# Kernel optimization log

Hardware: AMD Instinct MI355X
Metric: run time of the kernel (lower is better)

## Reference

```python
import jax, jax.numpy as jnp
import numpy as np

N = 50000   # nodes
E = 600000  # edges
F = 128     # num_features
H = 128     # hidden_channels
G = 64      # graphs in batch


def setup_inputs() -> dict:
    key = jax.random.key(0)
    ks = jax.random.split(key, 12)
    x = jax.random.normal(ks[0], (N, F), dtype=jnp.float32)
    edge_index = jax.random.randint(ks[1], (2, E), 0, N, dtype=jnp.int64)
    edge_mask = jax.random.randint(ks[2], (E,), 0, 3, dtype=jnp.int64)
    batch = jnp.sort(jax.random.randint(ks[3], (N,), 0, G, dtype=jnp.int64))
    s = 0.05
    W1 = jax.random.normal(ks[4], (F, H), dtype=jnp.float32) * s
    b1 = jnp.zeros((H,), jnp.float32)
    W2 = jax.random.normal(ks[5], (H, H), dtype=jnp.float32) * s
    b2 = jnp.zeros((H,), jnp.float32)
    W3 = jax.random.normal(ks[6], (H, H), dtype=jnp.float32) * s
    b3 = jnp.zeros((H,), jnp.float32)
    Wl = jax.random.normal(ks[7], (H, 1), dtype=jnp.float32) * s
    bl = jnp.zeros((1,), jnp.float32)
    return {"x": x, "edge_index": edge_index, "edge_mask": edge_mask, "batch": batch,
            "W1": W1, "b1": b1, "W2": W2, "b2": b2, "W3": W3, "b3": b3, "Wl": Wl, "bl": bl}


def gcn_conv(x, W, b, src, dst, ew, n):
    """PyG GCNConv: add self-loops, symmetric deg^-1/2 normalization.
    ew is a {0,1} per-edge weight implementing the dynamic edge subset
    (equivalent to edge_index[:, idx] subsetting, since masked edges
    contribute neither to degree nor to aggregation)."""
    h = x @ W                                                # [n, H]
    deg = jax.ops.segment_sum(ew, dst, num_segments=n) + 1.0  # self-loop adds 1
    dinv = jax.lax.rsqrt(deg)                                # deg^-1/2
    norm = ew * dinv[src] * dinv[dst]                        # per-edge coeff
    agg = jax.ops.segment_sum(h[src] * norm[:, None], dst, num_segments=n)
    agg = agg + h * (dinv * dinv)[:, None]                   # self-loop term 1/deg_i
    return agg + b


def reference(x, edge_index, edge_mask, batch, W1, b1, W2, b2, W3, b3, Wl, bl):
    src, dst = edge_index[0], edge_index[1]
    ones = jnp.ones((E,), x.dtype)
    h = jax.nn.relu(gcn_conv(x, W1, b1, src, dst, ones, N))
    m1 = (edge_mask == 1).astype(x.dtype)
    h = jax.nn.relu(gcn_conv(h, W2, b2, src, dst, m1, N))
    m2 = (edge_mask == 2).astype(x.dtype)
    h = gcn_conv(h, W3, b3, src, dst, m2, N)
    # global_mean_pool over batch ids
    sums = jax.ops.segment_sum(h, batch, num_segments=G)        # [G, H]
    cnt = jax.ops.segment_sum(jnp.ones((N,), h.dtype), batch, num_segments=G)
    pooled = sums / jnp.clip(cnt, 1.0)[:, None]
    # dropout(p=0.3) is identity in eval mode
    return pooled @ Wl + bl
```

## Files before the change

### kernel.cpp

```cpp
#include <hip/hip_runtime.h>

#define NN 50000
#define EE 600000
#define HH 128
#define GG 64
#define NPAD 50176
#define NR 196
#define RN 256
#define NSEC3 150528
#define NBLK3 588
#define EPB 3072
#define SCAP 3584
#define STAGB 7168

typedef __attribute__((ext_vector_type(8))) short short8;
typedef __attribute__((ext_vector_type(4))) float f32x4;
typedef __attribute__((ext_vector_type(4))) unsigned int u32x4;

__device__ __forceinline__ float bf2f(unsigned int u16) {
    union { unsigned int i; float f; } v; v.i = u16 << 16; return v.f;
}
__device__ __forceinline__ unsigned short f2bf(float f) {
    union { float f; unsigned int i; } v; v.f = f;
    unsigned int u = v.i;
    return (unsigned short)((u + 0x7FFFu + ((u >> 16) & 1u)) >> 16);
}

__device__ __forceinline__ short8 cvt8(f32x4 lo, f32x4 hi) {
    short8 r;
    r[0] = (short)f2bf(lo[0]); r[1] = (short)f2bf(lo[1]);
    r[2] = (short)f2bf(lo[2]); r[3] = (short)f2bf(lo[3]);
    r[4] = (short)f2bf(hi[0]); r[5] = (short)f2bf(hi[1]);
    r[6] = (short)f2bf(hi[2]); r[7] = (short)f2bf(hi[3]);
    return r;
}

__global__ __launch_bounds__(256) void k_part(const int* __restrict__ ei, const int* __restrict__ mask,
                                              int* __restrict__ scnt, unsigned int* __restrict__ sbuf) {
    __shared__ int bcnt[256];
    __shared__ int bcur[256];
    __shared__ int gbase[256];
    int t = threadIdx.x;
    int e0 = blockIdx.x * EPB;
    unsigned int pk[12]; int bin[12];
    bcnt[t] = 0; bcur[t] = 0;
    __syncthreads();
    #pragma unroll
    for (int j = 0; j < 12; j++) {
        int e = e0 + j * 256 + t;
        if (e < EE) {
            int s = ei[e];
            int d = ei[EE + e];
            int m = mask[e];
            pk[j] = (unsigned int)s | ((unsigned int)(d & 255) << 16) | ((unsigned int)m << 24);
            bin[j] = d >> 8;
            atomicAdd(&bcnt[bin[j]], 1);
        } else bin[j] = -1;
    }
    __syncthreads();
    int v = bcnt[t];
    gbase[t] = (v > 0) ? atomicAdd(&scnt[t], v) : 0;
    __syncthreads();
    #pragma unroll
    for (int j = 0; j < 12; j++) {
        if (bin[j] >= 0) {
            int b = bin[j];
            int pos = gbase[b] + atomicAdd(&bcur[b], 1);
            if (pos < SCAP) sbuf[(size_t)b * SCAP + pos] = pk[j];
        }
    }
}

__global__ __launch_bounds__(256) void k_cnt(const int* __restrict__ scnt,
                                             const unsigned int* __restrict__ sbuf,
                                             int* __restrict__ deg, float* __restrict__ dinv) {
    __shared__ int l0[RN], l1[RN], l2[RN];
    int t = threadIdx.x;
    int rng = blockIdx.x;
    l0[t] = 0; l1[t] = 0; l2[t] = 0;
    __syncthreads();
    int cnt = scnt[rng]; if (cnt > SCAP) cnt = SCAP;
    const unsigned int* sb = sbuf + (size_t)rng * SCAP;
    for (int i = t; i < cnt; i += 256) {
        unsigned int p = sb[i];
        int dl = (int)((p >> 16) & 255u);
        int m = (int)(p >> 24);
        atomicAdd(&l0[dl], 1);
        if (m == 1) atomicAdd(&l1[dl], 1);
        else if (m == 2) atomicAdd(&l2[dl], 1);
    }
    __syncthreads();
    int node = rng * RN + t;
    int a = l0[t], b = l1[t], c = l2[t];
    deg[node] = a;
    deg[NPAD + node] = b;
    deg[2 * NPAD + node] = c;
    dinv[node] = rsqrtf((float)a + 1.0f);
    dinv[NPAD + node] = rsqrtf((float)b + 1.0f);
    dinv[2 * NPAD + node] = rsqrtf((float)c + 1.0f);
}

__global__ __launch_bounds__(256) void k_scan1(const int* __restrict__ deg, int* __restrict__ btot) {
    __shared__ int ws[4];
    int t = threadIdx.x, lane = t & 63, w = t >> 6;
    int v = deg[blockIdx.x * 256 + t];
    #pragma unroll
    for (int off = 32; off > 0; off >>= 1) v += __shfl_xor(v, off);
    if (lane == 0) ws[w] = v;
    __syncthreads();
    if (t == 0) btot[blockIdx.x] = ws[0] + ws[1] + ws[2] + ws[3];
}

__global__ __launch_bounds__(1024) void k_scan2(const int* __restrict__ btot, int* __restrict__ boff) {
    __shared__ int ws[16];
    int t = threadIdx.x, lane = t & 63, w = t >> 6;
    int v = (t < NBLK3) ? btot[t] : 0;
    int x = v;
    #pragma unroll
    for (int off = 1; off < 64; off <<= 1) {
        int u = __shfl_up(x, off);
        if (lane >= off) x += u;
    }
    if (lane == 63) ws[w] = x;
    __syncthreads();
    int wo = 0;
    for (int k = 0; k < w; k++) wo += ws[k];
    if (t < NBLK3) boff[t] = wo + x - v;
}

__global__ __launch_bounds__(256) void k_scan3(const int* __restrict__ deg, const int* __restrict__ boff,
                                               int* __restrict__ rp) {
    __shared__ int ws[4];
    int t = threadIdx.x, lane = t & 63, w = t >> 6;
    int i = blockIdx.x * 256 + t;
    int v = deg[i];
    int x = v;
    #pragma unroll
    for (int off = 1; off < 64; off <<= 1) {
        int u = __shfl_up(x, off);
        if (lane >= off) x += u;
    }
    if (lane == 63) ws[w] = x;
    __syncthreads();
    int wo = 0;
    for (int k = 0; k < w; k++) wo += ws[k];
    int r = boff[blockIdx.x] + wo + x - v;
    rp[i] = r;
    if (i == NSEC3 - 1) rp[NSEC3] = r + v;
}

__global__ __launch_bounds__(256) void k_build(const int* __restrict__ scnt,
                                               const unsigned int* __restrict__ sbuf,
                                               const int* __restrict__ rp,
                                               unsigned short* __restrict__ csr) {
    __shared__ int lrp0[RN + 1], lrp1[RN + 1], lrp2[RN + 1];
    __shared__ int lc0[RN], lc1[RN], lc2[RN];
    __shared__ unsigned short stag[STAGB];
    int t = threadIdx.x;
    int rng = blockIdx.x;
    int vd0 = rng * RN;
    int base0 = rp[vd0], base1 = rp[NPAD + vd0], base2 = rp[2 * NPAD + vd0];
    for (int i = t; i < RN + 1; i += 256) {
        lrp0[i] = rp[vd0 + i] - base0;
        lrp1[i] = rp[NPAD + vd0 + i] - base1;
        lrp2[i] = rp[2 * NPAD + vd0 + i] - base2;
    }
    lc0[t] = 0; lc1[t] = 0; lc2[t] = 0;
    __syncthreads();
    int c0 = lrp0[RN], c1 = lrp1[RN], c2 = lrp2[RN];
    int cnt = scnt[rng]; if (cnt > SCAP) cnt = SCAP;
    const unsigned int* sb = sbuf + (size_t)rng * SCAP;
    for (int i = t; i < cnt; i += 256) {
        unsigned int p = sb[i];
        unsigned short src = (unsigned short)(p & 0xffffu);
        int dl = (int)((p >> 16) & 255u);
        int m = (int)(p >> 24);
        int sl = lrp0[dl] + atomicAdd(&lc0[dl], 1);
        stag[sl] = src;
        if (m == 1) { sl = c0 + lrp1[dl] + atomicAdd(&lc1[dl], 1); stag[sl] = src; }
        else if (m == 2) { sl = c0 + c1 + lrp2[dl] + atomicAdd(&lc2[dl], 1); stag[sl] = src; }
    }
    __syncthreads();
    for (int i = t; i < c0; i += 256) csr[base0 + i] = stag[i];
    for (int i = t; i < c1; i += 256) csr[base1 + i] = stag[c0 + i];
    for (int i = t; i < c2; i += 256) csr[base2 + i] = stag[c0 + c1 + i];
}

__global__ void k_wt3(const float* __restrict__ W1, const float* __restrict__ W2,
                      const float* __restrict__ W3, unsigned short* __restrict__ wt) {
    int i = blockIdx.x * 256 + threadIdx.x;
    int which = i >> 14;
    int r = i & 16383;
    const float* w = (which == 0) ? W1 : (which == 1) ? W2 : W3;
    int k = r >> 7, n = r & 127;
    wt[which * 16384 + n * HH + k] = f2bf(w[r]);
}

__global__ __launch_bounds__(256) void k_gemm_f(const float* __restrict__ in,
                                                const unsigned short* __restrict__ wt,
                                                unsigned short* __restrict__ h) {
    int w = threadIdx.x >> 6, lane = threadIdx.x & 63;
    int lr = lane & 15, lg = lane >> 4;
    int rowbase = (blockIdx.x * 4 + w) * 16;
    if (rowbase >= NN) return;
    int arow = rowbase + lr;
    const f32x4* ap = (const f32x4*)(in + (size_t)arow * HH + lg * 8);
    short8 a0 = cvt8(ap[0], ap[1]);
    short8 a1 = cvt8(ap[8], ap[9]);
    short8 a2 = cvt8(ap[16], ap[17]);
    short8 a3 = cvt8(ap[24], ap[25]);
    f32x4 acc[8];
    #pragma unroll
    for (int i = 0; i < 8; i++) acc[i] = (f32x4){0.f, 0.f, 0.f, 0.f};
    const unsigned short* wbase = wt + lr * HH + lg * 8;
    #pragma unroll
    for (int nc = 0; nc < 8; nc++) {
        const short8* bp = (const short8*)(wbase + nc * 16 * HH);
        short8 b0 = bp[0], b1 = bp[4], b2 = bp[8], b3 = bp[12];
        acc[nc] = __builtin_amdgcn_mfma_f32_16x16x32_bf16(a0, b0, acc[nc], 0, 0, 0);
        acc[nc] = __builtin_amdgcn_mfma_f32_16x16x32_bf16(a1, b1, acc[nc], 0, 0, 0);
        acc[nc] = __builtin_amdgcn_mfma_f32_16x16x32_bf16(a2, b2, acc[nc], 0, 0, 0);
        acc[nc] = __builtin_amdgcn_mfma_f32_16x16x32_bf16(a3, b3, acc[nc], 0, 0, 0);
    }
    int orow = rowbase + lg * 4;
    #pragma unroll
    for (int nc = 0; nc < 8; nc++) {
        #pragma unroll
        for (int j = 0; j < 4; j++) {
            h[(size_t)(orow + j) * HH + nc * 16 + lr] = f2bf(acc[nc][j]);
        }
    }
}

__global__ __launch_bounds__(256) void k_gemm_b(const unsigned short* __restrict__ in,
                                                const unsigned short* __restrict__ wt,
                                                unsigned short* __restrict__ h) {
    int w = threadIdx.x >> 6, lane = threadIdx.x & 63;
    int lr = lane & 15, lg = lane >> 4;
    int rowbase = (blockIdx.x * 4 + w) * 16;
    if (rowbase >= NN) return;
    int arow = rowbase + lr;
    const short8* ap = (const short8*)(in + (size_t)arow * HH + lg * 8);
    short8 a0 = ap[0], a1 = ap[4], a2 = ap[8], a3 = ap[12];
    f32x4 acc[8];
    #pragma unroll
    for (int i = 0; i < 8; i++) acc[i] = (f32x4){0.f, 0.f, 0.f, 0.f};
    const unsigned short* wbase = wt + lr * HH + lg * 8;
    #pragma unroll
    for (int nc = 0; nc < 8; nc++) {
        const short8* bp = (const short8*)(wbase + nc * 16 * HH);
        short8 b0 = bp[0], b1 = bp[4], b2 = bp[8], b3 = bp[12];
        acc[nc] = __builtin_amdgcn_mfma_f32_16x16x32_bf16(a0, b0, acc[nc], 0, 0, 0);
        acc[nc] = __builtin_amdgcn_mfma_f32_16x16x32_bf16(a1, b1, acc[nc], 0, 0, 0);
        acc[nc] = __builtin_amdgcn_mfma_f32_16x16x32_bf16(a2, b2, acc[nc], 0, 0, 0);
        acc[nc] = __builtin_amdgcn_mfma_f32_16x16x32_bf16(a3, b3, acc[nc], 0, 0, 0);
    }
    int orow = rowbase + lg * 4;
    #pragma unroll
    for (int nc = 0; nc < 8; nc++) {
        #pragma unroll
        for (int j = 0; j < 4; j++) {
            h[(size_t)(orow + j) * HH + nc * 16 + lr] = f2bf(acc[nc][j]);
        }
    }
}

__global__ __launch_bounds__(256) void k_agg(const unsigned short* __restrict__ h,
                                             const float* __restrict__ dinv,
                                             const unsigned short* __restrict__ csr,
                                             const int* __restrict__ rp,
                                             const float* __restrict__ bias,
                                             unsigned short* __restrict__ g,
                                             int relu) {
    int tid = threadIdx.x;
    int n = blockIdx.x * 16 + (tid >> 4);
    int l = tid & 15;
    float di = dinv[n];
    float c = di * di;
    u32x4 hv = *(const u32x4*)(h + (size_t)n * HH + l * 8);
    float acc0 = bf2f(hv[0] & 0xffffu) * c, acc1 = bf2f(hv[0] >> 16) * c;
    float acc2 = bf2f(hv[1] & 0xffffu) * c, acc3 = bf2f(hv[1] >> 16) * c;
    float acc4 = bf2f(hv[2] & 0xffffu) * c, acc5 = bf2f(hv[2] >> 16) * c;
    float acc6 = bf2f(hv[3] & 0xffffu) * c, acc7 = bf2f(hv[3] >> 16) * c;
    int e = rp[n], end = rp[n + 1];
    for (; e + 1 < end; e += 2) {
        int s0 = (int)csr[e];
        int s1 = (int)csr[e + 1];
        float w0 = dinv[s0] * di;
        float w1 = dinv[s1] * di;
        u32x4 v0 = *(const u32x4*)(h + (size_t)s0 * HH + l * 8);
        u32x4 v1 = *(const u32x4*)(h + (size_t)s1 * HH + l * 8);
        acc0 += w0 * bf2f(v0[0] & 0xffffu); acc1 += w0 * bf2f(v0[0] >> 16);
        acc2 += w0 * bf2f(v0[1] & 0xffffu); acc3 += w0 * bf2f(v0[1] >> 16);
        acc4 += w0 * bf2f(v0[2] & 0xffffu); acc5 += w0 * bf2f(v0[2] >> 16);
        acc6 += w0 * bf2f(v0[3] & 0xffffu); acc7 += w0 * bf2f(v0[3] >> 16);
        acc0 += w1 * bf2f(v1[0] & 0xffffu); acc1 += w1 * bf2f(v1[0] >> 16);
        acc2 += w1 * bf2f(v1[1] & 0xffffu); acc3 += w1 * bf2f(v1[1] >> 16);
        acc4 += w1 * bf2f(v1[2] & 0xffffu); acc5 += w1 * bf2f(v1[2] >> 16);
        acc6 += w1 * bf2f(v1[3] & 0xffffu); acc7 += w1 * bf2f(v1[3] >> 16);
    }
    if (e < end) {
        int s0 = (int)csr[e];
        float w0 = dinv[s0] * di;
        u32x4 v0 = *(const u32x4*)(h + (size_t)s0 * HH + l * 8);
        acc0 += w0 * bf2f(v0[0] & 0xffffu); acc1 += w0 * bf2f(v0[0] >> 16);
        acc2 += w0 * bf2f(v0[1] & 0xffffu); acc3 += w0 * bf2f(v0[1] >> 16);
        acc4 += w0 * bf2f(v0[2] & 0xffffu); acc5 += w0 * bf2f(v0[2] >> 16);
        acc6 += w0 * bf2f(v0[3] & 0xffffu); acc7 += w0 * bf2f(v0[3] >> 16);
    }
    f32x4 bp0 = *(const f32x4*)(bias + l * 8);
    f32x4 bp1 = *(const f32x4*)(bias + l * 8 + 4);
    acc0 += bp0[0]; acc1 += bp0[1]; acc2 += bp0[2]; acc3 += bp0[3];
    acc4 += bp1[0]; acc5 += bp1[1]; acc6 += bp1[2]; acc7 += bp1[3];
    if (relu) {
        acc0 = fmaxf(acc0, 0.f); acc1 = fmaxf(acc1, 0.f);
        acc2 = fmaxf(acc2, 0.f); acc3 = fmaxf(acc3, 0.f);
        acc4 = fmaxf(acc4, 0.f); acc5 = fmaxf(acc5, 0.f);
        acc6 = fmaxf(acc6, 0.f); acc7 = fmaxf(acc7, 0.f);
    }
    u32x4 o;
    o[0] = (unsigned int)f2bf(acc0) | ((unsigned int)f2bf(acc1) << 16);
    o[1] = (unsigned int)f2bf(acc2) | ((unsigned int)f2bf(acc3) << 16);
    o[2] = (unsigned int)f2bf(acc4) | ((unsigned int)f2bf(acc5) << 16);
    o[3] = (unsigned int)f2bf(acc6) | ((unsigned int)f2bf(acc7) << 16);
    *(u32x4*)(g + (size_t)n * HH + l * 8) = o;
}

__global__ __launch_bounds__(128) void k_pool_part(const unsigned short* __restrict__ g3,
                                                   const int* __restrict__ batch,
                                                   float* __restrict__ sums) {
    int t = threadIdx.x;
    int n0 = blockIdx.x * 64;
    int n1 = n0 + 64; if (n1 > NN) n1 = NN;
    int curb = batch[n0];
    float acc = 0.f;
    for (int n = n0; n < n1; n++) {
        int b = batch[n];
        if (b != curb) {
            atomicAdd(&sums[curb * HH + t], acc);
            acc = 0.f;
            curb = b;
        }
        acc += bf2f((unsigned int)g3[(size_t)n * HH + t]);
    }
    atomicAdd(&sums[curb * HH + t], acc);
}

__device__ __forceinline__ int lbound(const int* a, int n, int key) {
    int lo = 0, hi = n;
    while (lo < hi) { int mid = (lo + hi) >> 1; if (a[mid] < key) lo = mid + 1; else hi = mid; }
    return lo;
}

__global__ __launch_bounds__(128) void k_head(const float* __restrict__ sums,
                                              const int* __restrict__ batch,
                                              const float* __restrict__ Wl,
                                              const float* __restrict__ bl,
                                              float* __restrict__ out) {
    int gid = blockIdx.x;
    int t = threadIdx.x;
    int lo = lbound(batch, NN, gid);
    int hi = lbound(batch, NN, gid + 1);
    float cnt = (float)(hi - lo);
    if (cnt < 1.f) cnt = 1.f;
    float prod = (sums[gid * HH + t] / cnt) * Wl[t];
    __shared__ float sm[128];
    sm[t] = prod;
    __syncthreads();
    for (int off = 64; off > 0; off >>= 1) {
        if (t < off) sm[t] += sm[t + off];
        __syncthreads();
    }
    if (t == 0) out[gid] = sm[0] + bl[0];
}

extern "C" void kernel_launch(void* const* d_in, const int* in_sizes, int n_in,
                              void* d_out, int out_size, void* d_ws, size_t ws_size,
                              hipStream_t stream) {
    const float* x    = (const float*)d_in[0];
    const int*   ei   = (const int*)d_in[1];
    const int*   mask = (const int*)d_in[2];
    const int*   batch= (const int*)d_in[3];
    const float* W1   = (const float*)d_in[4];
    const float* b1   = (const float*)d_in[5];
    const float* W2   = (const float*)d_in[6];
    const float* b2   = (const float*)d_in[7];
    const float* W3   = (const float*)d_in[8];
    const float* b3   = (const float*)d_in[9];
    const float* Wl   = (const float*)d_in[10];
    const float* bl   = (const float*)d_in[11];
    float* out = (float*)d_out;

    char* ws = (char*)d_ws;
    unsigned short* g = (unsigned short*)(ws + 0);
    unsigned short* h = (unsigned short*)(ws + 12800000);
    unsigned short* wt1 = (unsigned short*)(ws + 25600000);
    unsigned short* wt2 = wt1 + 16384;
    unsigned short* wt3 = wt2 + 16384;
    int* deg   = (int*)(ws + 25698304);
    float* dinv= (float*)(ws + 26300416);
    int* rp    = (int*)(ws + 26902528);
    int* btot  = (int*)(ws + 27505152);
    int* boff  = (int*)(ws + 27509248);
    int* scnt  = (int*)(ws + 27513344);
    unsigned short* csr = (unsigned short*)(ws + 27514368);
    unsigned int* sbuf = (unsigned int*)(ws + 29914368);
    float* sums = (float*)(ws + 32724224);

    float* dinv1 = dinv;
    float* dinv2 = dinv + NPAD;
    float* dinv3 = dinv + 2 * NPAD;

    hipMemsetAsync(scnt, 0, (size_t)NR * sizeof(int), stream);
    hipMemsetAsync(sums, 0, (size_t)GG * HH * sizeof(float), stream);

    dim3 b256(256);
    k_part<<<dim3((EE + EPB - 1) / EPB), b256, 0, stream>>>(ei, mask, scnt, sbuf);
    k_cnt<<<dim3(NR), b256, 0, stream>>>(scnt, sbuf, deg, dinv);
    k_scan1<<<dim3(NBLK3), b256, 0, stream>>>(deg, btot);
    k_scan2<<<dim3(1), dim3(1024), 0, stream>>>(btot, boff);
    k_scan3<<<dim3(NBLK3), b256, 0, stream>>>(deg, boff, rp);
    k_build<<<dim3(NR), b256, 0, stream>>>(scnt, sbuf, rp, csr);

    k_wt3<<<dim3(192), b256, 0, stream>>>(W1, W2, W3, wt1);

    dim3 ggrid((NN + 63) / 64);
    dim3 agrid(NN / 16);

    k_gemm_f<<<ggrid, b256, 0, stream>>>(x, wt1, h);
    k_agg<<<agrid, b256, 0, stream>>>(h, dinv1, csr, rp, b1, g, 1);
    k_gemm_b<<<ggrid, b256, 0, stream>>>(g, wt2, h);
    k_agg<<<agrid, b256, 0, stream>>>(h, dinv2, csr, rp + NPAD, b2, g, 1);
    k_gemm_b<<<ggrid, b256, 0, stream>>>(g, wt3, h);
    k_agg<<<agrid, b256, 0, stream>>>(h, dinv3, csr, rp + 2 * NPAD, b3, g, 0);

    k_pool_part<<<dim3((NN + 63) / 64), dim3(128), 0, stream>>>(g, batch, sums);
    k_head<<<dim3(GG), dim3(128), 0, stream>>>(sums, batch, Wl, bl, out);
}
```

Baseline: 197.2 us.

## Fuse CSR scans into count/build kernels and fuse last aggregation with pooling

Range totals are now reduced inside k_cnt and the per-node exclusive scan is done inside k_build, which replaces three scan kernels with one small scan over range totals. The final aggregation now accumulates into pooled sums through shared-memory atomics, which removes the bf16 write of layer-3 output and the separate pooling kernel. Zeroing of sums moves into the weight-transpose kernel, which drops a memset. The edge loop is unrolled by 4 to issue more gathers in flight, at the cost of more registers and a heavier atomic epilogue.

```diff
diff --git a/kernel.cpp b/kernel.cpp
--- a/kernel.cpp
+++ b/kernel.cpp
@@ -8,7 +8,7 @@
 #define NR 196
 #define RN 256
 #define NSEC3 150528
-#define NBLK3 588
+#define NRT 588
 #define EPB 3072
 #define SCAP 3584
 #define STAGB 7168
@@ -73,9 +73,11 @@
 
 __global__ __launch_bounds__(256) void k_cnt(const int* __restrict__ scnt,
                                              const unsigned int* __restrict__ sbuf,
-                                             int* __restrict__ deg, float* __restrict__ dinv) {
+                                             int* __restrict__ deg, float* __restrict__ dinv,
+                                             int* __restrict__ rtot) {
     __shared__ int l0[RN], l1[RN], l2[RN];
-    int t = threadIdx.x;
+    __shared__ int red[12];
+    int t = threadIdx.x, lane = t & 63, w = t >> 6;
     int rng = blockIdx.x;
     l0[t] = 0; l1[t] = 0; l2[t] = 0;
     __syncthreads();
@@ -98,23 +100,22 @@
     dinv[node] = rsqrtf((float)a + 1.0f);
     dinv[NPAD + node] = rsqrtf((float)b + 1.0f);
     dinv[2 * NPAD + node] = rsqrtf((float)c + 1.0f);
-}
-
-__global__ __launch_bounds__(256) void k_scan1(const int* __restrict__ deg, int* __restrict__ btot) {
-    __shared__ int ws[4];
-    int t = threadIdx.x, lane = t & 63, w = t >> 6;
-    int v = deg[blockIdx.x * 256 + t];
-    #pragma unroll
-    for (int off = 32; off > 0; off >>= 1) v += __shfl_xor(v, off);
-    if (lane == 0) ws[w] = v;
-    __syncthreads();
-    if (t == 0) btot[blockIdx.x] = ws[0] + ws[1] + ws[2] + ws[3];
-}
-
-__global__ __launch_bounds__(1024) void k_scan2(const int* __restrict__ btot, int* __restrict__ boff) {
+    int sa = a, sb_ = b, sc = c;
+    #pragma unroll
+    for (int off = 32; off > 0; off >>= 1) {
+        sa += __shfl_xor(sa, off); sb_ += __shfl_xor(sb_, off); sc += __shfl_xor(sc, off);
+    }
+    if (lane == 0) { red[w] = sa; red[4 + w] = sb_; red[8 + w] = sc; }
+    __syncthreads();
+    if (t == 0) rtot[rng] = red[0] + red[1] + red[2] + red[3];
+    else if (t == 1) rtot[NR + rng] = red[4] + red[5] + red[6] + red[7];
+    else if (t == 2) rtot[2 * NR + rng] = red[8] + red[9] + red[10] + red[11];
+}
+
+__global__ __launch_bounds__(1024) void k_scanR(const int* __restrict__ rtot, int* __restrict__ roff) {
     __shared__ int ws[16];
     int t = threadIdx.x, lane = t & 63, w = t >> 6;
-    int v = (t < NBLK3) ? btot[t] : 0;
+    int v = (t < NRT) ? rtot[t] : 0;
     int x = v;
     #pragma unroll
     for (int off = 1; off < 64; off <<= 1) {
@@ -125,47 +126,41 @@
     __syncthreads();
     int wo = 0;
     for (int k = 0; k < w; k++) wo += ws[k];
-    if (t < NBLK3) boff[t] = wo + x - v;
-}
-
-__global__ __launch_bounds__(256) void k_scan3(const int* __restrict__ deg, const int* __restrict__ boff,
-                                               int* __restrict__ rp) {
-    __shared__ int ws[4];
-    int t = threadIdx.x, lane = t & 63, w = t >> 6;
-    int i = blockIdx.x * 256 + t;
-    int v = deg[i];
-    int x = v;
-    #pragma unroll
-    for (int off = 1; off < 64; off <<= 1) {
-        int u = __shfl_up(x, off);
-        if (lane >= off) x += u;
-    }
-    if (lane == 63) ws[w] = x;
-    __syncthreads();
-    int wo = 0;
-    for (int k = 0; k < w; k++) wo += ws[k];
-    int r = boff[blockIdx.x] + wo + x - v;
-    rp[i] = r;
-    if (i == NSEC3 - 1) rp[NSEC3] = r + v;
+    if (t < NRT) roff[t] = wo + x - v;
 }
 
 __global__ __launch_bounds__(256) void k_build(const int* __restrict__ scnt,
                                                const unsigned int* __restrict__ sbuf,
-                                               const int* __restrict__ rp,
+                                               const int* __restrict__ deg,
+                                               const int* __restrict__ roff,
+                                               int* __restrict__ rp,
                                                unsigned short* __restrict__ csr) {
     __shared__ int lrp0[RN + 1], lrp1[RN + 1], lrp2[RN + 1];
     __shared__ int lc0[RN], lc1[RN], lc2[RN];
+    __shared__ int wsum[12];
     __shared__ unsigned short stag[STAGB];
-    int t = threadIdx.x;
+    int t = threadIdx.x, lane = t & 63, w = t >> 6;
     int rng = blockIdx.x;
     int vd0 = rng * RN;
-    int base0 = rp[vd0], base1 = rp[NPAD + vd0], base2 = rp[2 * NPAD + vd0];
-    for (int i = t; i < RN + 1; i += 256) {
-        lrp0[i] = rp[vd0 + i] - base0;
-        lrp1[i] = rp[NPAD + vd0 + i] - base1;
-        lrp2[i] = rp[2 * NPAD + vd0 + i] - base2;
-    }
+    int d0 = deg[vd0 + t], d1 = deg[NPAD + vd0 + t], d2 = deg[2 * NPAD + vd0 + t];
+    int x0 = d0, x1 = d1, x2 = d2;
+    #pragma unroll
+    for (int off = 1; off < 64; off <<= 1) {
+        int u0 = __shfl_up(x0, off), u1 = __shfl_up(x1, off), u2 = __shfl_up(x2, off);
+        if (lane >= off) { x0 += u0; x1 += u1; x2 += u2; }
+    }
+    if (lane == 63) { wsum[w] = x0; wsum[4 + w] = x1; wsum[8 + w] = x2; }
+    __syncthreads();
+    int wo0 = 0, wo1 = 0, wo2 = 0;
+    for (int k = 0; k < w; k++) { wo0 += wsum[k]; wo1 += wsum[4 + k]; wo2 += wsum[8 + k]; }
+    int e0 = wo0 + x0 - d0, e1 = wo1 + x1 - d1, e2 = wo2 + x2 - d2;
+    lrp0[t] = e0; lrp1[t] = e1; lrp2[t] = e2;
+    if (t == 255) { lrp0[RN] = e0 + d0; lrp1[RN] = e1 + d1; lrp2[RN] = e2 + d2; }
     lc0[t] = 0; lc1[t] = 0; lc2[t] = 0;
+    int base0 = roff[rng], base1 = roff[NR + rng], base2 = roff[2 * NR + rng];
+    rp[vd0 + t] = base0 + e0;
+    rp[NPAD + vd0 + t] = base1 + e1;
+    rp[2 * NPAD + vd0 + t] = base2 + e2;
     __syncthreads();
     int c0 = lrp0[RN], c1 = lrp1[RN], c2 = lrp2[RN];
     int cnt = scnt[rng]; if (cnt > SCAP) cnt = SCAP;
@@ -186,9 +181,11 @@
     for (int i = t; i < c2; i += 256) csr[base2 + i] = stag[c0 + c1 + i];
 }
 
-__global__ void k_wt3(const float* __restrict__ W1, const float* __restrict__ W2,
-                      const float* __restrict__ W3, unsigned short* __restrict__ wt) {
+__global__ void k_wt3z(const float* __restrict__ W1, const float* __restrict__ W2,
+                       const float* __restrict__ W3, unsigned short* __restrict__ wt,
+                       float* __restrict__ sums) {
     int i = blockIdx.x * 256 + threadIdx.x;
+    if (i < GG * HH) sums[i] = 0.f;
     int which = i >> 14;
     int r = i & 16383;
     const float* w = (which == 0) ? W1 : (which == 1) ? W2 : W3;
@@ -265,85 +262,117 @@
     }
 }
 
+__device__ __forceinline__ void agg_edges(const unsigned short* __restrict__ h,
+                                          const float* __restrict__ dinv,
+                                          const unsigned short* __restrict__ csr,
+                                          int e, int end, float di, int l, float* acc) {
+    for (; e + 3 < end; e += 4) {
+        int s0 = (int)csr[e], s1 = (int)csr[e + 1], s2 = (int)csr[e + 2], s3 = (int)csr[e + 3];
+        float w0 = dinv[s0] * di, w1 = dinv[s1] * di, w2 = dinv[s2] * di, w3 = dinv[s3] * di;
+        u32x4 v0 = *(const u32x4*)(h + (size_t)s0 * HH + l * 8);
+        u32x4 v1 = *(const u32x4*)(h + (size_t)s1 * HH + l * 8);
+        u32x4 v2 = *(const u32x4*)(h + (size_t)s2 * HH + l * 8);
+        u32x4 v3 = *(const u32x4*)(h + (size_t)s3 * HH + l * 8);
+        #pragma unroll
+        for (int q = 0; q < 4; q++) {
+            acc[2*q]   += w0 * bf2f(v0[q] & 0xffffu); acc[2*q+1] += w0 * bf2f(v0[q] >> 16);
+            acc[2*q]   += w1 * bf2f(v1[q] & 0xffffu); acc[2*q+1] += w1 * bf2f(v1[q] >> 16);
+            acc[2*q]   += w2 * bf2f(v2[q] & 0xffffu); acc[2*q+1] += w2 * bf2f(v2[q] >> 16);
+            acc[2*q]   += w3 * bf2f(v3[q] & 0xffffu); acc[2*q+1] += w3 * bf2f(v3[q] >> 16);
+        }
+    }
+    for (; e < end; e++) {
+        int s0 = (int)csr[e];
+        float w0 = dinv[s0] * di;
+        u32x4 v0 = *(const u32x4*)(h + (size_t)s0 * HH + l * 8);
+        #pragma unroll
+        for (int q = 0; q < 4; q++) {
+            acc[2*q]   += w0 * bf2f(v0[q] & 0xffffu); acc[2*q+1] += w0 * bf2f(v0[q] >> 16);
+        }
+    }
+}
+
 __global__ __launch_bounds__(256) void k_agg(const unsigned short* __restrict__ h,
                                              const float* __restrict__ dinv,
                                              const unsigned short* __restrict__ csr,
                                              const int* __restrict__ rp,
                                              const float* __restrict__ bias,
-                                             unsigned short* __restrict__ g,
-                                             int relu) {
+                                             unsigned short* __restrict__ g) {
     int tid = threadIdx.x;
     int n = blockIdx.x * 16 + (tid >> 4);
     int l = tid & 15;
     float di = dinv[n];
     float c = di * di;
     u32x4 hv = *(const u32x4*)(h + (size_t)n * HH + l * 8);
-    float acc0 = bf2f(hv[0] & 0xffffu) * c, acc1 = bf2f(hv[0] >> 16) * c;
-    float acc2 = bf2f(hv[1] & 0xffffu) * c, acc3 = bf2f(hv[1] >> 16) * c;
-    float acc4 = bf2f(hv[2] & 0xffffu) * c, acc5 = bf2f(hv[2] >> 16) * c;
-    float acc6 = bf2f(hv[3] & 0xffffu) * c, acc7 = bf2f(hv[3] >> 16) * c;
-    int e = rp[n], end = rp[n + 1];
-    for (; e + 1 < end; e += 2) {
-        int s0 = (int)csr[e];
-        int s1 = (int)csr[e + 1];
-        float w0 = dinv[s0] * di;
-        float w1 = dinv[s1] * di;
-        u32x4 v0 = *(const u32x4*)(h + (size_t)s0 * HH + l * 8);
-        u32x4 v1 = *(const u32x4*)(h + (size_t)s1 * HH + l * 8);
-        acc0 += w0 * bf2f(v0[0] & 0xffffu); acc1 += w0 * bf2f(v0[0] >> 16);
-        acc2 += w0 * bf2f(v0[1] & 0xffffu); acc3 += w0 * bf2f(v0[1] >> 16);
-        acc4 += w0 * bf2f(v0[2] & 0xffffu); acc5 += w0 * bf2f(v0[2] >> 16);
-        acc6 += w0 * bf2f(v0[3] & 0xffffu); acc7 += w0 * bf2f(v0[3] >> 16);
-        acc0 += w1 * bf2f(v1[0] & 0xffffu); acc1 += w1 * bf2f(v1[0] >> 16);
-        acc2 += w1 * bf2f(v1[1] & 0xffffu); acc3 += w1 * bf2f(v1[1] >> 16);
-        acc4 += w1 * bf2f(v1[2] & 0xffffu); acc5 += w1 * bf2f(v1[2] >> 16);
-        acc6 += w1 * bf2f(v1[3] & 0xffffu); acc7 += w1 * bf2f(v1[3] >> 16);
-    }
-    if (e < end) {
-        int s0 = (int)csr[e];
-        float w0 = dinv[s0] * di;
-        u32x4 v0 = *(const u32x4*)(h + (size_t)s0 * HH + l * 8);
-        acc0 += w0 * bf2f(v0[0] & 0xffffu); acc1 += w0 * bf2f(v0[0] >> 16);
-        acc2 += w0 * bf2f(v0[1] & 0xffffu); acc3 += w0 * bf2f(v0[1] >> 16);
-        acc4 += w0 * bf2f(v0[2] & 0xffffu); acc5 += w0 * bf2f(v0[2] >> 16);
-        acc6 += w0 * bf2f(v0[3] & 0xffffu); acc7 += w0 * bf2f(v0[3] >> 16);
-    }
+    float acc[8];
+    #pragma unroll
+    for (int q = 0; q < 4; q++) {
+        acc[2*q] = bf2f(hv[q] & 0xffffu) * c;
+        acc[2*q+1] = bf2f(hv[q] >> 16) * c;
+    }
+    agg_edges(h, dinv, csr, rp[n], rp[n + 1], di, l, acc);
     f32x4 bp0 = *(const f32x4*)(bias + l * 8);
     f32x4 bp1 = *(const f32x4*)(bias + l * 8 + 4);
-    acc0 += bp0[0]; acc1 += bp0[1]; acc2 += bp0[2]; acc3 += bp0[3];
-    acc4 += bp1[0]; acc5 += bp1[1]; acc6 += bp1[2]; acc7 += bp1[3];
-    if (relu) {
-        acc0 = fmaxf(acc0, 0.f); acc1 = fmaxf(acc1, 0.f);
-        acc2 = fmaxf(acc2, 0.f); acc3 = fmaxf(acc3, 0.f);
-        acc4 = fmaxf(acc4, 0.f); acc5 = fmaxf(acc5, 0.f);
-        acc6 = fmaxf(acc6, 0.f); acc7 = fmaxf(acc7, 0.f);
-    }
+    acc[0] += bp0[0]; acc[1] += bp0[1]; acc[2] += bp0[2]; acc[3] += bp0[3];
+    acc[4] += bp1[0]; acc[5] += bp1[1]; acc[6] += bp1[2]; acc[7] += bp1[3];
+    #pragma unroll
+    for (int q = 0; q < 8; q++) acc[q] = fmaxf(acc[q], 0.f);
     u32x4 o;
-    o[0] = (unsigned int)f2bf(acc0) | ((unsigned int)f2bf(acc1) << 16);
-    o[1] = (unsigned int)f2bf(acc2) | ((unsigned int)f2bf(acc3) << 16);
-    o[2] = (unsigned int)f2bf(acc4) | ((unsigned int)f2bf(acc5) << 16);
-    o[3] = (unsigned int)f2bf(acc6) | ((unsigned int)f2bf(acc7) << 16);
+    #pragma unroll
+    for (int q = 0; q < 4; q++)
+        o[q] = (unsigned int)f2bf(acc[2*q]) | ((unsigned int)f2bf(acc[2*q+1]) << 16);
     *(u32x4*)(g + (size_t)n * HH + l * 8) = o;
 }
 
-__global__ __launch_bounds__(128) void k_pool_part(const unsigned short* __restrict__ g3,
-                                                   const int* __restrict__ batch,
-                                                   float* __restrict__ sums) {
-    int t = threadIdx.x;
-    int n0 = blockIdx.x * 64;
-    int n1 = n0 + 64; if (n1 > NN) n1 = NN;
-    int curb = batch[n0];
-    float acc = 0.f;
-    for (int n = n0; n < n1; n++) {
-        int b = batch[n];
-        if (b != curb) {
-            atomicAdd(&sums[curb * HH + t], acc);
-            acc = 0.f;
-            curb = b;
-        }
-        acc += bf2f((unsigned int)g3[(size_t)n * HH + t]);
-    }
-    atomicAdd(&sums[curb * HH + t], acc);
+__global__ __launch_bounds__(256) void k_aggpool(const unsigned short* __restrict__ h,
+                                                 const float* __restrict__ dinv,
+                                                 const unsigned short* __restrict__ csr,
+                                                 const int* __restrict__ rp,
+                                                 const float* __restrict__ bias,
+                                                 const int* __restrict__ batch,
+                                                 float* __restrict__ sums) {
+    __shared__ float lsum[4][HH];
+    __shared__ int lflag[4];
+    int tid = threadIdx.x;
+    int n = blockIdx.x * 16 + (tid >> 4);
+    int l = tid & 15;
+    for (int i = tid; i < 4 * HH; i += 256) ((float*)lsum)[i] = 0.f;
+    if (tid < 4) lflag[tid] = 0;
+    __syncthreads();
+    float di = dinv[n];
+    float c = di * di;
+    u32x4 hv = *(const u32x4*)(h + (size_t)n * HH + l * 8);
+    float acc[8];
+    #pragma unroll
+    for (int q = 0; q < 4; q++) {
+        acc[2*q] = bf2f(hv[q] & 0xffffu) * c;
+        acc[2*q+1] = bf2f(hv[q] >> 16) * c;
+    }
+    agg_edges(h, dinv, csr, rp[n], rp[n + 1], di, l, acc);
+    f32x4 bp0 = *(const f32x4*)(bias + l * 8);
+    f32x4 bp1 = *(const f32x4*)(bias + l * 8 + 4);
+    acc[0] += bp0[0]; acc[1] += bp0[1]; acc[2] += bp0[2]; acc[3] += bp0[3];
+    acc[4] += bp1[0]; acc[5] += bp1[1]; acc[6] += bp1[2]; acc[7] += bp1[3];
+    int b0 = batch[blockIdx.x * 16];
+    int bn = batch[n];
+    int rel = bn - b0;
+    if (rel < 4) {
+        lflag[rel] = 1;
+        #pragma unroll
+        for (int q = 0; q < 8; q++) atomicAdd(&lsum[rel][l * 8 + q], acc[q]);
+    } else {
+        #pragma unroll
+        for (int q = 0; q < 8; q++) atomicAdd(&sums[bn * HH + l * 8 + q], acc[q]);
+    }
+    __syncthreads();
+    #pragma unroll
+    for (int r = 0; r < 4; r++) {
+        if (lflag[r]) {
+            int gi = b0 + r;
+            for (int i = tid; i < HH; i += 256)
+                atomicAdd(&sums[gi * HH + i], lsum[r][i]);
+        }
+    }
 }
 
 __device__ __forceinline__ int lbound(const int* a, int n, int key) {
@@ -400,8 +429,8 @@
     int* deg   = (int*)(ws + 25698304);
     float* dinv= (float*)(ws + 26300416);
     int* rp    = (int*)(ws + 26902528);
-    int* btot  = (int*)(ws + 27505152);
-    int* boff  = (int*)(ws + 27509248);
+    int* rtot  = (int*)(ws + 27505152);
+    int* roff  = (int*)(ws + 27509248);
     int* scnt  = (int*)(ws + 27513344);
     unsigned short* csr = (unsigned short*)(ws + 27514368);
     unsigned int* sbuf = (unsigned int*)(ws + 29914368);
@@ -412,28 +441,24 @@
     float* dinv3 = dinv + 2 * NPAD;
 
     hipMemsetAsync(scnt, 0, (size_t)NR * sizeof(int), stream);
-    hipMemsetAsync(sums, 0, (size_t)GG * HH * sizeof(float), stream);
 
     dim3 b256(256);
     k_part<<<dim3((EE + EPB - 1) / EPB), b256, 0, stream>>>(ei, mask, scnt, sbuf);
-    k_cnt<<<dim3(NR), b256, 0, stream>>>(scnt, sbuf, deg, dinv);
-    k_scan1<<<dim3(NBLK3), b256, 0, stream>>>(deg, btot);
-    k_scan2<<<dim3(1), dim3(1024), 0, stream>>>(btot, boff);
-    k_scan3<<<dim3(NBLK3), b256, 0, stream>>>(deg, boff, rp);
-    k_build<<<dim3(NR), b256, 0, stream>>>(scnt, sbuf, rp, csr);
-
-    k_wt3<<<dim3(192), b256, 0, stream>>>(W1, W2, W3, wt1);
+    k_cnt<<<dim3(NR), b256, 0, stream>>>(scnt, sbuf, deg, dinv, rtot);
+    k_scanR<<<dim3(1), dim3(1024), 0, stream>>>(rtot, roff);
+    k_build<<<dim3(NR), b256, 0, stream>>>(scnt, sbuf, deg, roff, rp, csr);
+
+    k_wt3z<<<dim3(192), b256, 0, stream>>>(W1, W2, W3, wt1, sums);
 
     dim3 ggrid((NN + 63) / 64);
     dim3 agrid(NN / 16);
 
     k_gemm_f<<<ggrid, b256, 0, stream>>>(x, wt1, h);
-    k_agg<<<agrid, b256, 0, stream>>>(h, dinv1, csr, rp, b1, g, 1);
+    k_agg<<<agrid, b256, 0, stream>>>(h, dinv1, csr, rp, b1, g);
     k_gemm_b<<<ggrid, b256, 0, stream>>>(g, wt2, h);
-    k_agg<<<agrid, b256, 0, stream>>>(h, dinv2, csr, rp + NPAD, b2, g, 1);
+    k_agg<<<agrid, b256, 0, stream>>>(h, dinv2, csr, rp + NPAD, b2, g);
     k_gemm_b<<<ggrid, b256, 0, stream>>>(g, wt3, h);
-    k_agg<<<agrid, b256, 0, stream>>>(h, dinv3, csr, rp + 2 * NPAD, b3, g, 0);
-
-    k_pool_part<<<dim3((NN + 63) / 64), dim3(128), 0, stream>>>(g, batch, sums);
+    k_aggpool<<<agrid, b256, 0, stream>>>(h, dinv3, csr, rp + 2 * NPAD, b3, batch, sums);
+
     k_head<<<dim3(GG), dim3(128), 0, stream>>>(sums, batch, Wl, bl, out);
 }
```

Result: no change. 198.0 us (+0.4%).
